# Kernel optimization log

Hardware: AMD Instinct MI355X
Metric: run time of the kernel (lower is better)

The kernel has to match this reference:

```python
import jax, jax.numpy as jnp
import numpy as np

B, S, D, H, DK, CR = 4, 4096, 1024, 16, 64, 3


def setup_inputs() -> dict:
    rng = jax.random.key(0)
    ks = jax.random.split(rng, 13)
    sc = 1.0 / np.sqrt(D)
    u = lambda k, shape: jax.random.uniform(k, shape, jnp.float32, -sc, sc)
    return {
        "query": jax.random.normal(ks[0], (B, S, D), jnp.float32),
        "key": jax.random.normal(ks[1], (B, S, D), jnp.float32),
        "value": jax.random.normal(ks[2], (B, S, D), jnp.float32),
        "Wq": u(ks[3], (D, D)), "bq": u(ks[4], (D,)),
        "Wk": u(ks[5], (D, D)), "bk": u(ks[6], (D,)),
        "Wv": u(ks[7], (D, D)), "bv": u(ks[8], (D,)),
        "Wo": u(ks[9], (D, D)), "bo": u(ks[10], (D,)),
        "conv_w": u(ks[11], (D, D, CR)),  # Conv1d(D, D, kernel=CR, stride=CR)
        "conv_b": u(ks[12], (D,)),
    }


def _compress(x, w, b):
    # x: (B, L, D) -> strided conv over L -> (B, ceil-ish L/CR, D)
    y = jax.lax.conv_general_dilated(
        x.transpose(0, 2, 1), w, window_strides=(CR,), padding="VALID",
        dimension_numbers=("NCH", "OIH", "NCH"))
    return (y + b[None, :, None]).transpose(0, 2, 1)


def reference(query, key, value, Wq, bq, Wk, bk, Wv, bv, Wo, bo, conv_w, conv_b):
    # Source quirk: pad amount derived from d_model (last dim), applied to seq.
    pad = CR - D % CR  # = 2 here
    if pad < CR:
        key = jnp.pad(key, ((0, 0), (pad, 0), (0, 0)))
        value = jnp.pad(value, ((0, 0), (pad, 0), (0, 0)))
    key = _compress(key, conv_w, conv_b)
    value = _compress(value, conv_w, conv_b)

    def proj(x, W, bias):  # (B, L, D) -> (B, H, L, DK)
        return (x @ W.T + bias).reshape(x.shape[0], -1, H, DK).transpose(0, 2, 1, 3)

    q = proj(query, Wq, bq)
    k = proj(key, Wk, bk)
    v = proj(value, Wv, bv)

    scores = jnp.einsum("bhqd,bhkd->bhqk", q, k) / np.float32(np.sqrt(DK))
    attn = jax.nn.softmax(scores, axis=-1)  # dropout is identity at eval
    x = jnp.einsum("bhqk,bhkd->bhqd", attn, v)
    x = x.transpose(0, 2, 1, 3).reshape(query.shape[0], -1, H * DK)
    return x @ Wo.T + bo
```

## Files before the change

### kernel.cpp

```cpp
#include <hip/hip_runtime.h>


#define DM   1024
#define NH   16
#define DKH  64
#define BB   4
#define SQ   4096
#define LCC  1366
#define LCP  1408
#define SPAD 4098

#define QSC  0.18033688011f

typedef unsigned short u16;
using short8 = __attribute__((ext_vector_type(8))) short;
using f32x4  = __attribute__((ext_vector_type(4))) float;
using us4    = __attribute__((ext_vector_type(4))) unsigned short;
using us8    = __attribute__((ext_vector_type(8))) unsigned short;

__device__ __forceinline__ u16 f2bf(float f) {
    unsigned u = __float_as_uint(f);
    u += 0x7fffu + ((u >> 16) & 1u);
    return (u16)(u >> 16);
}

__device__ __forceinline__ void gl_lds16(const void* g, void* l) {
    __builtin_amdgcn_global_load_lds(
        (__attribute__((address_space(1))) unsigned int*)(uintptr_t)g,
        (__attribute__((address_space(3))) unsigned int*)l,
        16, 0, 0);
}

__global__ __launch_bounds__(256) void cast4_k(const float* __restrict__ in, u16* __restrict__ out,
                                               int n4, float scale) {
    int i = blockIdx.x * 256 + threadIdx.x;
    if (i >= n4) return;
    float4 v = ((const float4*)in)[i];
    us4 o;
    o[0] = f2bf(v.x * scale); o[1] = f2bf(v.y * scale);
    o[2] = f2bf(v.z * scale); o[3] = f2bf(v.w * scale);
    ((us4*)out)[i] = o;
}

__global__ __launch_bounds__(256) void cast4w_k(
    const float* __restrict__ w0, const float* __restrict__ w1,
    const float* __restrict__ w2, const float* __restrict__ w3,
    u16* __restrict__ o0, u16* __restrict__ o1, u16* __restrict__ o2, u16* __restrict__ o3,
    float qsc) {
    int z = blockIdx.z;
    const float* in = (z == 0) ? w0 : (z == 1) ? w1 : (z == 2) ? w2 : w3;
    u16* out        = (z == 0) ? o0 : (z == 1) ? o1 : (z == 2) ? o2 : o3;
    float scale     = (z == 0) ? qsc : 1.0f;
    int i = blockIdx.x * 256 + threadIdx.x;
    float4 v = ((const float4*)in)[i];
    us4 o;
    o[0] = f2bf(v.x * scale); o[1] = f2bf(v.y * scale);
    o[2] = f2bf(v.z * scale); o[3] = f2bf(v.w * scale);
    ((us4*)out)[i] = o;
}

__global__ __launch_bounds__(256) void cast_pad2_k(const float* __restrict__ in0, u16* __restrict__ out0,
                                                   const float* __restrict__ in1, u16* __restrict__ out1) {
    const float* in = blockIdx.z ? in1 : in0;
    u16* out        = blockIdx.z ? out1 : out0;
    int i = blockIdx.x * 256 + threadIdx.x;
    const int n4 = BB * SPAD * DM / 4;
    if (i >= n4) return;
    int e   = i * 4;
    int b   = e / (SPAD * DM);
    int rem = e - b * (SPAD * DM);
    int s   = rem >> 10;
    int d   = rem & (DM - 1);
    us4 o = {0, 0, 0, 0};
    if (s >= 2) {
        float4 v = *(const float4*)(in + (size_t)(b * SQ + (s - 2)) * DM + d);
        o[0] = f2bf(v.x); o[1] = f2bf(v.y); o[2] = f2bf(v.z); o[3] = f2bf(v.w);
    }
    ((us4*)out)[i] = o;
}

__global__ __launch_bounds__(256) void permcast_conv_k(const float* __restrict__ cw, u16* __restrict__ wc2) {
    int i = blockIdx.x * 256 + threadIdx.x;
    const int n4 = DM * DM * 3 / 4;
    if (i >= n4) return;
    int e   = i * 4;
    int o   = e / 3072;
    int rem = e - o * 3072;
    int r   = rem >> 10;
    int ii  = rem & 1023;
    us4 q;
    #pragma unroll
    for (int t = 0; t < 4; ++t) q[t] = f2bf(cw[(size_t)(o * DM + ii + t) * 3 + r]);
    ((us4*)wc2)[i] = q;
}

__global__ __launch_bounds__(256) void transpose_v_k(const u16* __restrict__ vp, u16* __restrict__ vt) {
    __shared__ u16 t[64 * 65];
    const int tid = threadIdx.x;
    const int j0 = blockIdx.x * 64;
    const int bh = blockIdx.y, b = bh >> 4, h = bh & 15;
    #pragma unroll
    for (int it = 0; it < 2; ++it) {
        int cc = tid + it * 256;
        int j = cc >> 3, d0 = (cc & 7) * 8;
        int jj = j0 + j;
        us8 v = {0, 0, 0, 0, 0, 0, 0, 0};
        if (jj < LCC) v = *(const us8*)(vp + (size_t)(b * LCC + jj) * DM + h * DKH + d0);
        #pragma unroll
        for (int q = 0; q < 8; ++q) t[(d0 + q) * 65 + j] = v[q];
    }
    __syncthreads();
    #pragma unroll
    for (int it = 0; it < 2; ++it) {
        int cc = tid + it * 256;
        int d = cc >> 3, q0 = (cc & 7) * 8;
        us8 v;
        #pragma unroll
        for (int q = 0; q < 8; ++q) {
            int cp = q0 + q;
            int ks = cp >> 5, qd = (cp >> 3) & 3, j = cp & 7;
            int k  = (ks + 2 * (j >> 2)) * 16 + qd * 4 + (j & 3);
            v[q] = t[d * 65 + k];
        }
        *(us8*)(vt + (size_t)(bh * DKH + d) * LCP + j0 + q0) = v;
    }
}

__global__ __launch_bounds__(256, 2) void gemm_mfma_k(
    const u16* __restrict__ A0, const u16* __restrict__ B0, const float* __restrict__ bias0, void* __restrict__ C0,
    const u16* __restrict__ A1, const u16* __restrict__ B1, const float* __restrict__ bias1, void* __restrict__ C1,
    int N, int K, int cf32, float bscale)
{
    const u16* A      = blockIdx.z ? A1 : A0;
    const u16* Bw     = blockIdx.z ? B1 : B0;
    const float* bias = blockIdx.z ? bias1 : bias0;
    void* C           = blockIdx.z ? C1 : C0;

    __shared__ u16 lds[2 * 16384];
    const int tid = threadIdx.x, wave = tid >> 6, lane = tid & 63;
    const int quad = lane >> 4, l15 = lane & 15;
    const int n0 = blockIdx.y * 128, o0 = blockIdx.x * 128;
    const int wm = (wave >> 1) * 64, wn = (wave & 1) * 64;
    const int srow = (lane >> 3), sc8 = (lane & 7);

    f32x4 acc[4][4];
    #pragma unroll
    for (int a = 0; a < 4; ++a)
        #pragma unroll
        for (int b = 0; b < 4; ++b)
            #pragma unroll
            for (int r = 0; r < 4; ++r) acc[a][b][r] = 0.0f;

    auto stage = [&](int kt, u16* base) {
        #pragma unroll
        for (int i = 0; i < 4; ++i) {
            int is  = wave * 4 + i;
            int row = is * 8 + srow;
            int c   = sc8 ^ (row & 7);
            int ra  = n0 + row; if (ra > N - 1) ra = N - 1;
            gl_lds16(A  + (size_t)ra * K + kt + c * 8,          base + is * 512 + lane * 8);
            gl_lds16(Bw + (size_t)(o0 + row) * K + kt + c * 8,  base + 8192 + is * 512 + lane * 8);
        }
    };

    stage(0, lds);
    int cur = 0;
    const int nk = K >> 6;
    for (int ki = 0; ki < nk; ++ki) {
        __syncthreads();
        if (ki + 1 < nk) stage((ki + 1) << 6, lds + (cur ^ 1) * 16384);
        const u16* As = lds + cur * 16384;
        const u16* Bs = As + 8192;
        #pragma unroll
        for (int ks = 0; ks < 2; ++ks) {
            short8 af[4], bf[4];
            #pragma unroll
            for (int mi = 0; mi < 4; ++mi) {
                int m = wm + mi * 16 + l15;
                int c = (ks * 4 + quad) ^ (m & 7);
                af[mi] = *(const short8*)(As + m * 64 + c * 8);
            }
            #pragma unroll
            for (int nj = 0; nj < 4; ++nj) {
                int n = wn + nj * 16 + l15;
                int c = (ks * 4 + quad) ^ (n & 7);
                bf[nj] = *(const short8*)(Bs + n * 64 + c * 8);
            }
            #pragma unroll
            for (int mi = 0; mi < 4; ++mi)
                #pragma unroll
                for (int nj = 0; nj < 4; ++nj)
                    acc[mi][nj] = __builtin_amdgcn_mfma_f32_16x16x32_bf16(af[mi], bf[nj], acc[mi][nj], 0, 0, 0);
        }
        cur ^= 1;
    }
    #pragma unroll
    for (int mi = 0; mi < 4; ++mi) {
        #pragma unroll
        for (int r = 0; r < 4; ++r) {
            int n = n0 + wm + mi * 16 + quad * 4 + r;
            if (n < N) {
                #pragma unroll
                for (int nj = 0; nj < 4; ++nj) {
                    int o = o0 + wn + nj * 16 + l15;
                    float v = acc[mi][nj][r] + bias[o] * bscale;
                    if (cf32) ((float*)C)[(size_t)n * DM + o] = v;
                    else      ((u16*)C)[(size_t)n * DM + o] = f2bf(v);
                }
            }
        }
    }
}

__global__ __launch_bounds__(256, 3) void attn_mfma_k(
    const u16* __restrict__ qp, const u16* __restrict__ kp,
    const u16* __restrict__ vt, u16* __restrict__ xo)
{
    __shared__ u16 lds[4 * 4096];
    const int tid = threadIdx.x, wave = tid >> 6, lane = tid & 63;
    const int quad = lane >> 4, l15 = lane & 15;
    const int bh = blockIdx.y, b = bh >> 4, h = bh & 15;
    const int s0 = blockIdx.x * 128;
    const int wq = wave * 32;
    const int srow = lane >> 3, sc8 = lane & 7;

    #pragma unroll
    for (int i = 0; i < 4; ++i) {
        int is = wave * 4 + i;
        int row = is * 8 + srow;
        int c = sc8 ^ (row & 7);
        gl_lds16(qp + (size_t)(b * SQ + s0 + row) * DM + h * DKH + c * 8,
                 lds + is * 512 + lane * 8);
    }
    __syncthreads();
    short8 qfr[2][2];
    #pragma unroll
    for (int qg = 0; qg < 2; ++qg) {
        int m = wq + qg * 16 + l15;
        #pragma unroll
        for (int ks = 0; ks < 2; ++ks) {
            int c = (ks * 4 + quad) ^ (m & 7);
            qfr[qg][ks] = *(const short8*)(lds + m * 64 + c * 8);
        }
    }
    __syncthreads();

    f32x4 oacc[2][4], lacc[2];
    #pragma unroll
    for (int a = 0; a < 2; ++a) {
        #pragma unroll
        for (int r = 0; r < 4; ++r) lacc[a][r] = 0.0f;
        #pragma unroll
        for (int d = 0; d < 4; ++d)
            #pragma unroll
            for (int r = 0; r < 4; ++r) oacc[a][d][r] = 0.0f;
    }
    union { unsigned u[4]; short8 s; } onesu;
    #pragma unroll
    for (int i = 0; i < 4; ++i) onesu.u[i] = 0x3f803f80u;
    const short8 ones = onesu.s;

    #pragma unroll
    for (int i = 0; i < 2; ++i) {
        int is = wave * 2 + i;
        int row = is * 8 + srow;
        int c = sc8 ^ (row & 7);
        int j = row; if (j > LCC - 1) j = LCC - 1;
        gl_lds16(kp + (size_t)(b * LCC + j) * DM + h * DKH + c * 8, lds + is * 512 + lane * 8);
        gl_lds16(vt + (size_t)(bh * DKH + row) * LCP + c * 8,       lds + 4096 + is * 512 + lane * 8);
    }

    int cur = 0;
    for (int t = 0; t < 22; ++t) {
        const int j0 = t * 64;
        __syncthreads();
        if (t < 21) {
            int nj0 = j0 + 64;
            u16* base = lds + (cur ^ 1) * 8192;
            #pragma unroll
            for (int i = 0; i < 2; ++i) {
                int is = wave * 2 + i;
                int row = is * 8 + srow;
                int c = sc8 ^ (row & 7);
                int j = nj0 + row; if (j > LCC - 1) j = LCC - 1;
                gl_lds16(kp + (size_t)(b * LCC + j) * DM + h * DKH + c * 8, base + is * 512 + lane * 8);
                gl_lds16(vt + (size_t)(bh * DKH + row) * LCP + nj0 + c * 8, base + 4096 + is * 512 + lane * 8);
            }
        }
        const u16* Kb = lds + cur * 8192;
        const u16* Vb = Kb + 4096;

        f32x4 sc[2][4];
        #pragma unroll
        for (int a = 0; a < 2; ++a)
            #pragma unroll
            for (int n = 0; n < 4; ++n)
                #pragma unroll
                for (int r = 0; r < 4; ++r) sc[a][n][r] = 0.0f;
        __builtin_amdgcn_s_setprio(1);
        #pragma unroll
        for (int ks = 0; ks < 2; ++ks) {
            short8 kfr[4];
            #pragma unroll
            for (int nj = 0; nj < 4; ++nj) {
                int n = nj * 16 + l15;
                int c = (ks * 4 + quad) ^ (n & 7);
                kfr[nj] = *(const short8*)(Kb + n * 64 + c * 8);
            }
            #pragma unroll
            for (int qg = 0; qg < 2; ++qg)
                #pragma unroll
                for (int nj = 0; nj < 4; ++nj)
                    sc[qg][nj] = __builtin_amdgcn_mfma_f32_16x16x32_bf16(kfr[nj], qfr[qg][ks], sc[qg][nj], 0, 0, 0);
        }
        __builtin_amdgcn_s_setprio(0);

        const bool tail = (j0 + 64 > LCC);
        #pragma unroll
        for (int qg = 0; qg < 2; ++qg) {
            #pragma unroll
            for (int nj = 0; nj < 4; ++nj) {
                #pragma unroll
                for (int r = 0; r < 4; ++r) {
                    float p = __builtin_amdgcn_exp2f(sc[qg][nj][r]);
                    if (tail && (j0 + nj * 16 + quad * 4 + r) >= LCC) p = 0.0f;
                    sc[qg][nj][r] = p;
                }
            }
        }
        short8 pa[2][2];
        #pragma unroll
        for (int qg = 0; qg < 2; ++qg) {
            #pragma unroll
            for (int ks = 0; ks < 2; ++ks) {
                unsigned w0, w1, w2, w3;
                asm("v_cvt_pk_bf16_f32 %0, %1, %2" : "=v"(w0) : "v"(sc[qg][ks][0]),     "v"(sc[qg][ks][1]));
                asm("v_cvt_pk_bf16_f32 %0, %1, %2" : "=v"(w1) : "v"(sc[qg][ks][2]),     "v"(sc[qg][ks][3]));
                asm("v_cvt_pk_bf16_f32 %0, %1, %2" : "=v"(w2) : "v"(sc[qg][ks + 2][0]), "v"(sc[qg][ks + 2][1]));
                asm("v_cvt_pk_bf16_f32 %0, %1, %2" : "=v"(w3) : "v"(sc[qg][ks + 2][2]), "v"(sc[qg][ks + 2][3]));
                union { unsigned u[4]; short8 s; } cv;
                cv.u[0] = w0; cv.u[1] = w1; cv.u[2] = w2; cv.u[3] = w3;
                pa[qg][ks] = cv.s;
            }
        }
        __builtin_amdgcn_s_setprio(1);
        #pragma unroll
        for (int ks = 0; ks < 2; ++ks) {
            short8 vfr[4];
            #pragma unroll
            for (int dj = 0; dj < 4; ++dj) {
                int d = dj * 16 + l15;
                int c = (ks * 4 + quad) ^ (d & 7);
                vfr[dj] = *(const short8*)(Vb + d * 64 + c * 8);
            }
            #pragma unroll
            for (int qg = 0; qg < 2; ++qg) {
                #pragma unroll
                for (int dj = 0; dj < 4; ++dj)
                    oacc[qg][dj] = __builtin_amdgcn_mfma_f32_16x16x32_bf16(pa[qg][ks], vfr[dj], oacc[qg][dj], 0, 0, 0);
                lacc[qg] = __builtin_amdgcn_mfma_f32_16x16x32_bf16(pa[qg][ks], ones, lacc[qg], 0, 0, 0);
            }
        }
        __builtin_amdgcn_s_setprio(0);
        cur ^= 1;
    }

    #pragma unroll
    for (int qg = 0; qg < 2; ++qg) {
        #pragma unroll
        for (int r = 0; r < 4; ++r) {
            float inv = 1.0f / lacc[qg][r];
            int s = s0 + wq + qg * 16 + quad * 4 + r;
            #pragma unroll
            for (int dj = 0; dj < 4; ++dj)
                xo[(size_t)(b * SQ + s) * DM + h * DKH + dj * 16 + l15] = f2bf(oacc[qg][dj][r] * inv);
        }
    }
}

extern "C" void kernel_launch(void* const* d_in, const int* in_sizes, int n_in,
                              void* d_out, int out_size, void* d_ws, size_t ws_size,
                              hipStream_t stream)
{
    const float* query  = (const float*)d_in[0];
    const float* key    = (const float*)d_in[1];
    const float* value  = (const float*)d_in[2];
    const float* Wq     = (const float*)d_in[3];
    const float* bq     = (const float*)d_in[4];
    const float* Wk     = (const float*)d_in[5];
    const float* bk     = (const float*)d_in[6];
    const float* Wv     = (const float*)d_in[7];
    const float* bv     = (const float*)d_in[8];
    const float* Wo     = (const float*)d_in[9];
    const float* bo     = (const float*)d_in[10];
    const float* conv_w = (const float*)d_in[11];
    const float* conv_b = (const float*)d_in[12];
    float* out = (float*)d_out;

    u16* p = (u16*)d_ws;
    auto alloc = [&](size_t n) { u16* r = p; p += (n + 127) & ~(size_t)127; return r; };
    u16* qbf  = alloc((size_t)BB * SQ * DM);
    u16* kpad = alloc((size_t)BB * SPAD * DM);
    u16* vpad = alloc((size_t)BB * SPAD * DM);
    u16* wqb  = alloc((size_t)DM * DM);
    u16* wkb  = alloc((size_t)DM * DM);
    u16* wvb  = alloc((size_t)DM * DM);
    u16* wob  = alloc((size_t)DM * DM);
    u16* wc2b = alloc((size_t)DM * DM * 3);
    u16* kc   = alloc((size_t)BB * LCC * DM);
    u16* vc   = alloc((size_t)BB * LCC * DM);
    u16* kpj  = alloc((size_t)BB * LCC * DM);
    u16* vpj  = alloc((size_t)BB * LCC * DM);
    u16* qprj = alloc((size_t)BB * SQ * DM);
    u16* vtb  = alloc((size_t)BB * NH * DKH * LCP);
    u16* xo   = alloc((size_t)BB * SQ * DM);

    const int NC = BB * LCC;
    const int NS = BB * SQ;

    cast4_k<<<dim3(NS * DM / 4 / 256), 256, 0, stream>>>(query, qbf, NS * DM / 4, 1.0f);
    cast_pad2_k<<<dim3((BB * SPAD * DM / 4 + 255) / 256, 1, 2), 256, 0, stream>>>(key, kpad, value, vpad);
    cast4w_k<<<dim3(DM * DM / 4 / 256, 1, 4), 256, 0, stream>>>(Wq, Wk, Wv, Wo, wqb, wkb, wvb, wob, QSC);
    permcast_conv_k<<<dim3(DM * DM * 3 / 4 / 256), 256, 0, stream>>>(conv_w, wc2b);

    gemm_mfma_k<<<dim3(8, 43, 2), 256, 0, stream>>>(kpad, wc2b, conv_b, kc,
                                                    vpad, wc2b, conv_b, vc, NC, 3072, 0, 1.0f);

    gemm_mfma_k<<<dim3(8, 128, 1), 256, 0, stream>>>(qbf, wqb, bq, qprj,
                                                     qbf, wqb, bq, qprj, NS, DM, 0, QSC);
    gemm_mfma_k<<<dim3(8, 43, 2), 256, 0, stream>>>(kc, wkb, bk, kpj,
                                                    vc, wvb, bv, vpj, NC, DM, 0, 1.0f);

    transpose_v_k<<<dim3(22, BB * NH), 256, 0, stream>>>(vpj, vtb);

    attn_mfma_k<<<dim3(SQ / 128, BB * NH), 256, 0, stream>>>(qprj, kpj, vtb, xo);

    gemm_mfma_k<<<dim3(8, 128, 1), 256, 0, stream>>>(xo, wob, bo, out,
                                                     xo, wob, bo, out, NS, DM, 1, 1.0f);
}
```

Before: 644.5 us.

## Remap blocks across XCDs and single-buffer GEMM LDS for higher occupancy

Adds an XCD-aware block index remap to both the GEMM and attention kernels so that neighbouring tiles land on the same XCD and share its L2. The GEMM drops its double-buffered LDS staging in favour of one buffer with a sync before and after compute, which halves LDS use and lets the launch bound rise from 2 to 3 blocks per CU. The trade is that global-to-LDS loads no longer overlap with MFMA work inside a block; the extra resident blocks are expected to hide that latency instead.

```diff
diff --git a/kernel.cpp b/kernel.cpp
--- a/kernel.cpp
+++ b/kernel.cpp
@@ -29,6 +29,11 @@
         (__attribute__((address_space(1))) unsigned int*)(uintptr_t)g,
         (__attribute__((address_space(3))) unsigned int*)l,
         16, 0, 0);
+}
+
+__device__ __forceinline__ int xcd_remap(int i, int T) {
+    if (T & 7) return i;
+    return (i & 7) * (T >> 3) + (i >> 3);
 }
 
 __global__ __launch_bounds__(256) void cast4_k(const float* __restrict__ in, u16* __restrict__ out,
@@ -126,22 +131,30 @@
     }
 }
 
-__global__ __launch_bounds__(256, 2) void gemm_mfma_k(
+__global__ __launch_bounds__(256, 3) void gemm_mfma_k(
     const u16* __restrict__ A0, const u16* __restrict__ B0, const float* __restrict__ bias0, void* __restrict__ C0,
     const u16* __restrict__ A1, const u16* __restrict__ B1, const float* __restrict__ bias1, void* __restrict__ C1,
     int N, int K, int cf32, float bscale)
 {
-    const u16* A      = blockIdx.z ? A1 : A0;
-    const u16* Bw     = blockIdx.z ? B1 : B0;
-    const float* bias = blockIdx.z ? bias1 : bias0;
-    void* C           = blockIdx.z ? C1 : C0;
-
-    __shared__ u16 lds[2 * 16384];
+    int T  = gridDim.x * gridDim.y * gridDim.z;
+    int i0 = blockIdx.x + gridDim.x * (blockIdx.y + gridDim.y * blockIdx.z);
+    int j  = xcd_remap(i0, T);
+    int bx = j % gridDim.x;
+    int rem2 = j / gridDim.x;
+    int by = rem2 % gridDim.y;
+    int bz = rem2 / gridDim.y;
+
+    const u16* A      = bz ? A1 : A0;
+    const u16* Bw     = bz ? B1 : B0;
+    const float* bias = bz ? bias1 : bias0;
+    void* C           = bz ? C1 : C0;
+
+    __shared__ u16 As[128 * 64];
+    __shared__ u16 Bs[128 * 64];
     const int tid = threadIdx.x, wave = tid >> 6, lane = tid & 63;
     const int quad = lane >> 4, l15 = lane & 15;
-    const int n0 = blockIdx.y * 128, o0 = blockIdx.x * 128;
+    const int n0 = by * 128, o0 = bx * 128;
     const int wm = (wave >> 1) * 64, wn = (wave & 1) * 64;
-    const int srow = (lane >> 3), sc8 = (lane & 7);
 
     f32x4 acc[4][4];
     #pragma unroll
@@ -151,26 +164,20 @@
             #pragma unroll
             for (int r = 0; r < 4; ++r) acc[a][b][r] = 0.0f;
 
-    auto stage = [&](int kt, u16* base) {
+    const int srow = (lane >> 3);
+    const int sc8  = (lane & 7);
+
+    for (int kt = 0; kt < K; kt += 64) {
         #pragma unroll
         for (int i = 0; i < 4; ++i) {
             int is  = wave * 4 + i;
             int row = is * 8 + srow;
             int c   = sc8 ^ (row & 7);
             int ra  = n0 + row; if (ra > N - 1) ra = N - 1;
-            gl_lds16(A  + (size_t)ra * K + kt + c * 8,          base + is * 512 + lane * 8);
-            gl_lds16(Bw + (size_t)(o0 + row) * K + kt + c * 8,  base + 8192 + is * 512 + lane * 8);
-        }
-    };
-
-    stage(0, lds);
-    int cur = 0;
-    const int nk = K >> 6;
-    for (int ki = 0; ki < nk; ++ki) {
+            gl_lds16(A  + (size_t)ra * K + kt + c * 8,          As + is * 512 + lane * 8);
+            gl_lds16(Bw + (size_t)(o0 + row) * K + kt + c * 8,  Bs + is * 512 + lane * 8);
+        }
         __syncthreads();
-        if (ki + 1 < nk) stage((ki + 1) << 6, lds + (cur ^ 1) * 16384);
-        const u16* As = lds + cur * 16384;
-        const u16* Bs = As + 8192;
         #pragma unroll
         for (int ks = 0; ks < 2; ++ks) {
             short8 af[4], bf[4];
@@ -192,7 +199,7 @@
                 for (int nj = 0; nj < 4; ++nj)
                     acc[mi][nj] = __builtin_amdgcn_mfma_f32_16x16x32_bf16(af[mi], bf[nj], acc[mi][nj], 0, 0, 0);
         }
-        cur ^= 1;
+        __syncthreads();
     }
     #pragma unroll
     for (int mi = 0; mi < 4; ++mi) {
@@ -219,8 +226,15 @@
     __shared__ u16 lds[4 * 4096];
     const int tid = threadIdx.x, wave = tid >> 6, lane = tid & 63;
     const int quad = lane >> 4, l15 = lane & 15;
-    const int bh = blockIdx.y, b = bh >> 4, h = bh & 15;
-    const int s0 = blockIdx.x * 128;
+
+    int T  = gridDim.x * gridDim.y;
+    int i0 = blockIdx.x + gridDim.x * blockIdx.y;
+    int j5 = xcd_remap(i0, T);
+    int bxs = j5 % gridDim.x;
+    int bh  = j5 / gridDim.x;
+
+    const int b = bh >> 4, h = bh & 15;
+    const int s0 = bxs * 128;
     const int wq = wave * 32;
     const int srow = lane >> 3, sc8 = lane & 7;
 
```

Measured after the change: 560.1 us. -13.1%, faster.
